# Optimization experiments

Hardware: AMD Instinct MI355X
Metric: run time of the kernel (lower is better)

Reference implementation:

```python
import jax, jax.numpy as jnp
import numpy as np

N, E, DIN, HID, HEADS = 50000, 1600000, 256, 256, 4
C = (HID // 2) // HEADS  # 32 per-head channels; HEADS*C = HID//2 per direction
NEG_SLOPE = 0.2
BN_EPS = 1e-5


def setup_inputs() -> dict:
    key = jax.random.key(0)
    ks = jax.random.split(key, 16)
    s = lambda k, shp: (jax.random.normal(k, shp, jnp.float32) * 0.05)
    return {
        "x": jax.random.normal(ks[0], (N, DIN), jnp.float32),
        "edge_index": jax.random.randint(ks[1], (2, E), 0, N, jnp.int32),
        # forward-direction GATConv params
        "W_f": s(ks[2], (DIN, HEADS * C)),
        "a_src_f": s(ks[3], (HEADS, C)),
        "a_dst_f": s(ks[4], (HEADS, C)),
        "b_f": jnp.zeros((HEADS * C,), jnp.float32),
        # backward-direction GATConv params
        "W_b": s(ks[5], (DIN, HEADS * C)),
        "a_src_b": s(ks[6], (HEADS, C)),
        "a_dst_b": s(ks[7], (HEADS, C)),
        "b_b": jnp.zeros((HEADS * C,), jnp.float32),
        # fusion linear + batchnorm (eval mode)
        "W_fuse": s(ks[8], (HID, HID)),
        "b_fuse": jnp.zeros((HID,), jnp.float32),
        "gamma": jnp.ones((HID,), jnp.float32),
        "beta": jnp.zeros((HID,), jnp.float32),
        "run_mean": jnp.zeros((HID,), jnp.float32),
        "run_var": jnp.ones((HID,), jnp.float32),
    }


def _gat(x, W, a_src, a_dst, b, src, dst):
    # x: [N, DIN]; src/dst: [E'] (self loops included)
    xl = (x @ W).reshape(N, HEADS, C)               # per-head projected features
    al = jnp.einsum("nhc,hc->nh", xl, a_src)        # [N, H]
    ar = jnp.einsum("nhc,hc->nh", xl, a_dst)        # [N, H]
    e = jax.nn.leaky_relu(al[src] + ar[dst], NEG_SLOPE)  # [E', H]
    # segment softmax over edges sharing the same destination node
    m = jax.ops.segment_max(e, dst, num_segments=N)      # [N, H]
    w = jnp.exp(e - m[dst])
    den = jax.ops.segment_sum(w, dst, num_segments=N)    # [N, H]
    alpha = w / (den[dst] + 1e-16)                       # [E', H]
    msg = xl[src] * alpha[..., None]                     # [E', H, C]
    out = jax.ops.segment_sum(msg, dst, num_segments=N)  # [N, H, C]
    return out.reshape(N, HEADS * C) + b


def reference(x, edge_index, W_f, a_src_f, a_dst_f, b_f, W_b, a_src_b, a_dst_b, b_b,
              W_fuse, b_fuse, gamma, beta, run_mean, run_var):
    loop = jnp.arange(N, dtype=edge_index.dtype)
    src = jnp.concatenate([edge_index[0], loop])  # add self loops (PyG default)
    dst = jnp.concatenate([edge_index[1], loop])
    fwd = _gat(x, W_f, a_src_f, a_dst_f, b_f, src, dst)   # [N, HID//2]
    bwd = _gat(x, W_b, a_src_b, a_dst_b, b_b, dst, src)   # reversed edges
    h = jnp.concatenate([fwd, bwd], axis=1) @ W_fuse + b_fuse  # [N, HID]
    h = (h - run_mean) * jax.lax.rsqrt(run_var + BN_EPS) * gamma + beta
    return jax.nn.relu(h)
```

## Files before the change

### kernel.cpp

```cpp
#include <hip/hip_runtime.h>

#define N_NODES 50000
#define N_EDGES 1600000
#define NEG_SLOPE 0.2f

#define NBUCK 98
#define BSH 9
#define NPB 512
#define CHUNK 6400
#define NBLK 250

typedef __attribute__((ext_vector_type(8))) short short8;
typedef __attribute__((ext_vector_type(4))) float floatx4;

__device__ __forceinline__ unsigned short f2bf(float f) {
  unsigned u = __float_as_uint(f);
  u += 0x7FFFu + ((u >> 16) & 1);
  return (unsigned short)(u >> 16);
}
__device__ __forceinline__ float bflo(unsigned u) { return __uint_as_float(u << 16); }
__device__ __forceinline__ float bfhi(unsigned u) { return __uint_as_float(u & 0xFFFF0000u); }

__global__ __launch_bounds__(256) void k_setup(
    const int* __restrict__ ei, int* __restrict__ blockhist,
    const float* __restrict__ W_f, const float* __restrict__ W_b,
    const float* __restrict__ W_fu,
    unsigned short* __restrict__ Bt1, unsigned short* __restrict__ Bt2,
    const float* __restrict__ x, unsigned short* __restrict__ Xsp)
{
  const int tid = threadIdx.x;
  if (blockIdx.x >= NBLK + 256) {
    const unsigned gid = (unsigned)(blockIdx.x - (NBLK + 256)) * 256u + tid;
    const unsigned row = gid >> 6, c = (gid & 63) * 4;
    float4 v = *(const float4*)(x + (size_t)row * 256 + c);
    unsigned short h0 = f2bf(v.x), h1 = f2bf(v.y), h2 = f2bf(v.z), h3 = f2bf(v.w);
    float l0 = v.x - __uint_as_float((unsigned)h0 << 16);
    float l1 = v.y - __uint_as_float((unsigned)h1 << 16);
    float l2 = v.z - __uint_as_float((unsigned)h2 << 16);
    float l3 = v.w - __uint_as_float((unsigned)h3 << 16);
    *(ushort4*)(Xsp + (size_t)row * 512 + c) = make_ushort4(h0, h1, h2, h3);
    *(ushort4*)(Xsp + (size_t)row * 512 + 256 + c) =
        make_ushort4(f2bf(l0), f2bf(l1), f2bf(l2), f2bf(l3));
    return;
  }
  if (blockIdx.x >= NBLK) {
    const int k = blockIdx.x - NBLK;
    float w1 = (tid < 128) ? W_f[k * 128 + tid] : W_b[k * 128 + (tid - 128)];
    Bt1[(size_t)tid * 256 + k] = f2bf(w1);
    Bt2[(size_t)tid * 256 + k] = f2bf(W_fu[k * 256 + tid]);
    return;
  }
  __shared__ int hist[2 * NBUCK];
  const int blk = blockIdx.x;
  for (int i = tid; i < 2 * NBUCK; i += 256) hist[i] = 0;
  __syncthreads();
  const int e0 = blk * CHUNK;
  for (int e = e0 + tid; e < e0 + CHUNK; e += 256) {
    int s = ei[e];
    int d = ei[N_EDGES + e];
    atomicAdd(&hist[d >> BSH], 1);
    atomicAdd(&hist[NBUCK + (s >> BSH)], 1);
  }
  __syncthreads();
  for (int i = tid; i < 2 * NBUCK; i += 256)
    blockhist[i * NBLK + blk] = hist[i];
}

__global__ __launch_bounds__(256) void k_rowscan(const int* __restrict__ blockhist,
                                                 int* __restrict__ blockoffs, int* __restrict__ bucktotal) {
  const int i = blockIdx.x;
  const int t = threadIdx.x;
  __shared__ int s[256];
  int v = (t < NBLK) ? blockhist[i * NBLK + t] : 0;
  s[t] = v;
  __syncthreads();
  for (int off = 1; off < 256; off <<= 1) {
    int u = (t >= off) ? s[t - off] : 0;
    __syncthreads();
    s[t] += u;
    __syncthreads();
  }
  if (t < NBLK) blockoffs[i * NBLK + t] = s[t] - v;
  if (t == 255) bucktotal[i] = s[255];
}

__global__ __launch_bounds__(256) void k_buckscan(const int* __restrict__ bucktotal,
                                                  int* __restrict__ buckbase, int* rpf, int* rpb) {
  __shared__ int s[256];
  const int t = threadIdx.x;
  int v = (t < 2 * NBUCK) ? bucktotal[t] : 0;
  s[t] = v;
  __syncthreads();
  for (int off = 1; off < 256; off <<= 1) {
    int u = (t >= off) ? s[t - off] : 0;
    __syncthreads();
    s[t] += u;
    __syncthreads();
  }
  if (t < 2 * NBUCK) {
    const int dir = (t >= NBUCK) ? 1 : 0;
    const int b = t - dir * NBUCK;
    const int sub = dir ? s[NBUCK - 1] : 0;
    buckbase[dir * (NBUCK + 1) + b] = s[t] - v - sub;
    if (b == NBUCK - 1) buckbase[dir * (NBUCK + 1) + NBUCK] = s[t] - sub;
  }
  if (t == 0) { rpf[N_NODES] = N_EDGES + N_NODES; rpb[N_NODES] = N_EDGES + N_NODES; }
}

__global__ __launch_bounds__(256) void k_stage(const int* __restrict__ ei,
                                               const int* __restrict__ blockoffs,
                                               const int* __restrict__ buckbase,
                                               uint2* __restrict__ staging) {
  __shared__ int cur[2 * NBUCK];
  const int blk = blockIdx.x, tid = threadIdx.x;
  for (int i = tid; i < 2 * NBUCK; i += 256) {
    int dir = (i >= NBUCK) ? 1 : 0;
    int b = i - dir * NBUCK;
    cur[i] = blockoffs[i * NBLK + blk] + buckbase[dir * (NBUCK + 1) + b];
  }
  __syncthreads();
  uint2* st0 = staging;
  uint2* st1 = staging + N_EDGES;
  const int e0 = blk * CHUNK;
  for (int e = e0 + tid; e < e0 + CHUNK; e += 256) {
    int s = ei[e];
    int d = ei[N_EDGES + e];
    int p = atomicAdd(&cur[d >> BSH], 1);
    st0[p] = make_uint2((unsigned)d, (unsigned)s);
    int q = atomicAdd(&cur[NBUCK + (s >> BSH)], 1);
    st1[q] = make_uint2((unsigned)s, (unsigned)d);
  }
}

__global__ __launch_bounds__(512) void k_bin(const uint2* __restrict__ staging,
                                             const int* __restrict__ buckbase,
                                             int* __restrict__ rpf, int* __restrict__ rpb,
                                             int* __restrict__ adjf, int* __restrict__ adjb) {
  const int b = blockIdx.x, dir = blockIdx.y, tid = threadIdx.x;
  const int node0 = b << BSH;
  const int nn = min(NPB, N_NODES - node0);
  const uint2* st = staging + (size_t)dir * N_EDGES;
  int* rp  = dir ? rpb : rpf;
  int* adj = dir ? adjb : adjf;
  const int beg = buckbase[dir * (NBUCK + 1) + b];
  const int end = buckbase[dir * (NBUCK + 1) + b + 1];

  __shared__ int cnt[NPB];
  __shared__ int wpart[8];
  cnt[tid] = 0;
  __syncthreads();
  for (int jj = beg + tid; jj < end; jj += 512)
    atomicAdd(&cnt[st[jj].x - node0], 1);
  __syncthreads();
  const int deg1 = (tid < nn) ? cnt[tid] + 1 : 0;
  int v = deg1;
  const int wl = tid & 63;
#pragma unroll
  for (int off = 1; off < 64; off <<= 1) {
    int u = __shfl_up(v, off, 64);
    if (wl >= off) v += u;
  }
  if (wl == 63) wpart[tid >> 6] = v;
  __syncthreads();
  int pre = 0;
#pragma unroll
  for (int w = 0; w < 7; ++w)
    if (w < (tid >> 6)) pre += wpart[w];
  const int excl = v + pre - deg1;
  if (tid < nn) {
    int r = beg + node0 + excl;
    rp[node0 + tid] = r;
    adj[r] = node0 + tid;
    cnt[tid] = r + 1;
  }
  __syncthreads();
  for (int jj = beg + tid; jj < end; jj += 512) {
    uint2 kv = st[jj];
    int p = atomicAdd(&cnt[kv.x - node0], 1);
    adj[p] = (int)kv.y;
  }
}

#define LDA 40

__global__ __launch_bounds__(256) void k_mm(
    const unsigned short* __restrict__ A, int M,
    const unsigned short* __restrict__ Bt,
    unsigned short* __restrict__ D0, unsigned short* __restrict__ D1,
    float* __restrict__ Df, int mode,
    const float* __restrict__ bias, const float* __restrict__ gamma,
    const float* __restrict__ beta, const float* __restrict__ mean,
    const float* __restrict__ var)
{
  __shared__ __align__(16) unsigned short As[128 * LDA];
  __shared__ __align__(16) unsigned short Bs[128 * LDA];
  const int tid = threadIdx.x;
  const int m0 = blockIdx.x * 128, col0 = blockIdx.y * 128;
  const int wave = tid >> 6, lane = tid & 63;
  const int wm = wave >> 1, wn = wave & 1;
  const int lm = lane & 15, quad = lane >> 4;

  floatx4 acc[4][4];
#pragma unroll
  for (int i = 0; i < 4; ++i)
#pragma unroll
    for (int j = 0; j < 4; ++j) acc[i][j] = (floatx4){0.f, 0.f, 0.f, 0.f};

  for (int it = 0; it < 16; ++it) {
    const int kk0 = it * 32;
    const int kbase = kk0 & 255;
    __syncthreads();
#pragma unroll
    for (int q = 0; q < 2; ++q) {
      int idx = q * 256 + tid;
      int r = idx >> 2, c8 = (idx & 3) * 8;
      ulonglong2 z; z.x = 0; z.y = 0;
      if (m0 + r < M) z = *(const ulonglong2*)(A + (size_t)(m0 + r) * 512 + kk0 + c8);
      *(ulonglong2*)&As[r * LDA + c8] = z;
    }
#pragma unroll
    for (int q = 0; q < 2; ++q) {
      int idx = q * 256 + tid;
      int nc = idx >> 2, c8 = (idx & 3) * 8;
      ulonglong2 z = *(const ulonglong2*)(Bt + (size_t)(col0 + nc) * 256 + kbase + c8);
      *(ulonglong2*)&Bs[nc * LDA + c8] = z;
    }
    __syncthreads();
    short8 a[4], b[4];
#pragma unroll
    for (int i = 0; i < 4; ++i)
      a[i] = *(const short8*)&As[(wm * 64 + i * 16 + lm) * LDA + quad * 8];
#pragma unroll
    for (int j = 0; j < 4; ++j)
      b[j] = *(const short8*)&Bs[(wn * 64 + j * 16 + lm) * LDA + quad * 8];
#pragma unroll
    for (int i = 0; i < 4; ++i)
#pragma unroll
      for (int j = 0; j < 4; ++j)
        acc[i][j] = __builtin_amdgcn_mfma_f32_16x16x32_bf16(a[i], b[j], acc[i][j], 0, 0, 0);
  }

  if (mode == 0) {
    unsigned short* C = (col0 >= 128) ? D1 : D0;
#pragma unroll
    for (int i = 0; i < 4; ++i) {
#pragma unroll
      for (int j = 0; j < 4; ++j) {
        int lc = (wn * 64 + j * 16 + lm);
#pragma unroll
        for (int reg = 0; reg < 4; ++reg) {
          int gr = m0 + wm * 64 + i * 16 + quad * 4 + reg;
          if (gr < M) C[(size_t)gr * 128 + lc] = f2bf(acc[i][j][reg]);
        }
      }
    }
  } else {
#pragma unroll
    for (int j = 0; j < 4; ++j) {
      int gc = col0 + wn * 64 + j * 16 + lm;
      float bi = bias[gc], mu = mean[gc], iv = rsqrtf(var[gc] + 1e-5f);
      float ga = gamma[gc], be = beta[gc];
#pragma unroll
      for (int i = 0; i < 4; ++i) {
#pragma unroll
        for (int reg = 0; reg < 4; ++reg) {
          int gr = m0 + wm * 64 + i * 16 + quad * 4 + reg;
          if (gr < M) {
            float v = acc[i][j][reg] + bi;
            v = (v - mu) * iv * ga + be;
            Df[(size_t)gr * 256 + gc] = fmaxf(v, 0.f);
          }
        }
      }
    }
  }
}

__global__ __launch_bounds__(256) void k_scores(
    const unsigned short* __restrict__ Xf, const unsigned short* __restrict__ Xb,
    const float* __restrict__ asf, const float* __restrict__ adf,
    const float* __restrict__ asb, const float* __restrict__ adb,
    float* __restrict__ ALf, float* __restrict__ ARf,
    float* __restrict__ ALb, float* __restrict__ ARb)
{
  const int wave = threadIdx.x >> 6, lane = threadIdx.x & 63;
  const int n = blockIdx.x * 4 + wave;
  const int hh = lane >> 5;
  const int c = lane & 31;
  float v0 = bflo((unsigned)Xf[(size_t)n * 128 + lane]);
  float v1 = bflo((unsigned)Xf[(size_t)n * 128 + 64 + lane]);
  float v2 = bflo((unsigned)Xb[(size_t)n * 128 + lane]);
  float v3 = bflo((unsigned)Xb[(size_t)n * 128 + 64 + lane]);
  float s0 = v0 * asf[hh * 32 + c],       d0 = v0 * adf[hh * 32 + c];
  float s1 = v1 * asf[(2 + hh) * 32 + c], d1 = v1 * adf[(2 + hh) * 32 + c];
  float s2 = v2 * asb[hh * 32 + c],       d2 = v2 * adb[hh * 32 + c];
  float s3 = v3 * asb[(2 + hh) * 32 + c], d3 = v3 * adb[(2 + hh) * 32 + c];
#pragma unroll
  for (int off = 16; off > 0; off >>= 1) {
    s0 += __shfl_xor(s0, off, 32); d0 += __shfl_xor(d0, off, 32);
    s1 += __shfl_xor(s1, off, 32); d1 += __shfl_xor(d1, off, 32);
    s2 += __shfl_xor(s2, off, 32); d2 += __shfl_xor(d2, off, 32);
    s3 += __shfl_xor(s3, off, 32); d3 += __shfl_xor(d3, off, 32);
  }
  if (c == 0) {
    ALf[n * 4 + hh] = s0;     ARf[n * 4 + hh] = d0;
    ALf[n * 4 + 2 + hh] = s1; ARf[n * 4 + 2 + hh] = d1;
    ALb[n * 4 + hh] = s2;     ARb[n * 4 + hh] = d2;
    ALb[n * 4 + 2 + hh] = s3; ARb[n * 4 + 2 + hh] = d3;
  }
}

__global__ __launch_bounds__(256) void k_agg(
    const uint2* __restrict__ Xf, const uint2* __restrict__ Xb,
    const int* __restrict__ rpf, const int* __restrict__ adjf,
    const int* __restrict__ rpb, const int* __restrict__ adjb,
    const float* __restrict__ ALf, const float* __restrict__ ARf,
    const float* __restrict__ ALb, const float* __restrict__ ARb,
    const float* __restrict__ bf, const float* __restrict__ bb,
    unsigned* __restrict__ Hsp)
{
  const int dir = blockIdx.y;
  const int wave = threadIdx.x >> 6;
  const int n = blockIdx.x * 4 + wave;
  const uint2* X = dir ? Xb : Xf;
  const int* rp  = dir ? rpb : rpf;
  const int* adj = dir ? adjb : adjf;
  const float* AL = dir ? ALb : ALf;
  const float* AR = dir ? ARb : ARf;
  const float* bias = dir ? bb : bf;
  const int lane = threadIdx.x & 63;
  const int sub = lane >> 5;
  const int t = lane & 31;
  const unsigned h = (unsigned)(t >> 3);
  const float arn = AR[((unsigned)n << 2) | h];
  const int beg = rp[n], end = rp[n + 1];
  const int iters = (end - beg + 1) >> 1;
  const int endm1 = end - 1;
  float a0 = 0.f, a1 = 0.f, a2 = 0.f, a3 = 0.f, den = 0.f;
  int j = beg + sub;
#pragma unroll 4
  for (int it = 0; it < iters; ++it, j += 2) {
    int jj = min(j, endm1);
    int nb = adj[jj];
    float al = AL[((unsigned)nb << 2) | h];
    uint2 u = X[(unsigned)nb * 32u + (unsigned)t];
    float e = al + arn;
    e = fmaxf(e, e * NEG_SLOPE);
    float w = __expf(e);
    w = (j <= endm1) ? w : 0.f;
    den += w;
    a0 = fmaf(w, bflo(u.x), a0);
    a1 = fmaf(w, bfhi(u.x), a1);
    a2 = fmaf(w, bflo(u.y), a2);
    a3 = fmaf(w, bfhi(u.y), a3);
  }
  a0 += __shfl_xor(a0, 32); a1 += __shfl_xor(a1, 32);
  a2 += __shfl_xor(a2, 32); a3 += __shfl_xor(a3, 32);
  den += __shfl_xor(den, 32);
  if (sub == 0) {
    float inv = 1.f / (den + 1e-16f);
    float4 bv = *(const float4*)(bias + 4 * t);
    float v0 = a0 * inv + bv.x, v1 = a1 * inv + bv.y;
    float v2 = a2 * inv + bv.z, v3 = a3 * inv + bv.w;
    unsigned short h0 = f2bf(v0), h1 = f2bf(v1), h2 = f2bf(v2), h3 = f2bf(v3);
    float l0 = v0 - __uint_as_float((unsigned)h0 << 16);
    float l1 = v1 - __uint_as_float((unsigned)h1 << 16);
    float l2 = v2 - __uint_as_float((unsigned)h2 << 16);
    float l3 = v3 - __uint_as_float((unsigned)h3 << 16);
    uint2 hiw, low;
    hiw.x = ((unsigned)h1 << 16) | h0;
    hiw.y = ((unsigned)h3 << 16) | h2;
    low.x = ((unsigned)f2bf(l1) << 16) | f2bf(l0);
    low.y = ((unsigned)f2bf(l3) << 16) | f2bf(l2);
    unsigned base = (unsigned)n * 256u + (unsigned)dir * 64u + 2u * (unsigned)t;
    *(uint2*)(Hsp + base) = hiw;
    *(uint2*)(Hsp + base + 128u) = low;
  }
}


extern "C" void kernel_launch(void* const* d_in, const int* in_sizes, int n_in,
                              void* d_out, int out_size, void* d_ws, size_t ws_size,
                              hipStream_t stream) {
  const float* x    = (const float*)d_in[0];
  const int*   ei   = (const int*)d_in[1];
  const float* W_f  = (const float*)d_in[2];
  const float* asf  = (const float*)d_in[3];
  const float* adf  = (const float*)d_in[4];
  const float* b_f  = (const float*)d_in[5];
  const float* W_b  = (const float*)d_in[6];
  const float* asb  = (const float*)d_in[7];
  const float* adb  = (const float*)d_in[8];
  const float* b_b  = (const float*)d_in[9];
  const float* W_fu = (const float*)d_in[10];
  const float* b_fu = (const float*)d_in[11];
  const float* gam  = (const float*)d_in[12];
  const float* bet  = (const float*)d_in[13];
  const float* mean = (const float*)d_in[14];
  const float* var  = (const float*)d_in[15];
  float* out = (float*)d_out;

  char* base = (char*)d_ws;
  size_t off = 0;
  auto alloc = [&](size_t bytes) {
    void* p = base + off;
    off = (off + bytes + 255) & ~(size_t)255;
    return p;
  };
  unsigned* Hsp          = (unsigned*)alloc((size_t)N_NODES * 256 * 4);
  unsigned short* Xsp    = (unsigned short*)Hsp;
  unsigned short* Xf     = (unsigned short*)alloc((size_t)N_NODES * 128 * 2);
  unsigned short* Xb     = (unsigned short*)alloc((size_t)N_NODES * 128 * 2);
  unsigned short* Bt1    = (unsigned short*)alloc((size_t)256 * 256 * 2);
  unsigned short* Bt2    = (unsigned short*)alloc((size_t)256 * 256 * 2);
  float* ALf  = (float*)alloc((size_t)N_NODES * 4 * 4);
  float* ARf  = (float*)alloc((size_t)N_NODES * 4 * 4);
  float* ALb  = (float*)alloc((size_t)N_NODES * 4 * 4);
  float* ARb  = (float*)alloc((size_t)N_NODES * 4 * 4);
  int* rpf    = (int*)alloc((size_t)(N_NODES + 1) * 4);
  int* rpb    = (int*)alloc((size_t)(N_NODES + 1) * 4);
  int* adjf   = (int*)alloc((size_t)(N_EDGES + N_NODES) * 4);
  int* adjb   = (int*)alloc((size_t)(N_EDGES + N_NODES) * 4);
  int* blockhist = (int*)alloc((size_t)2 * NBUCK * NBLK * 4);
  int* blockoffs = (int*)alloc((size_t)2 * NBUCK * NBLK * 4);
  int* bucktotal = (int*)alloc((size_t)2 * NBUCK * 4);
  int* buckbase  = (int*)alloc((size_t)2 * (NBUCK + 1) * 4);
  uint2* staging = (uint2*)alloc((size_t)2 * N_EDGES * 8);
  (void)ws_size; (void)in_sizes; (void)n_in; (void)out_size;

  const int SPLITB = (N_NODES * 64) / 256;
  k_setup<<<NBLK + 256 + SPLITB, 256, 0, stream>>>(ei, blockhist, W_f, W_b, W_fu,
                                                   Bt1, Bt2, x, Xsp);
  k_rowscan<<<2 * NBUCK, 256, 0, stream>>>(blockhist, blockoffs, bucktotal);
  k_buckscan<<<1, 256, 0, stream>>>(bucktotal, buckbase, rpf, rpb);
  k_stage<<<NBLK, 256, 0, stream>>>(ei, blockoffs, buckbase, staging);
  k_bin<<<dim3(NBUCK, 2), 512, 0, stream>>>(staging, buckbase, rpf, rpb, adjf, adjb);

  const int MB = (N_NODES + 127) / 128;
  k_mm<<<dim3(MB, 2), 256, 0, stream>>>(Xsp, N_NODES, Bt1, Xf, Xb, nullptr, 0,
                                        nullptr, nullptr, nullptr, nullptr, nullptr);
  k_scores<<<N_NODES / 4, 256, 0, stream>>>(Xf, Xb, asf, adf, asb, adb,
                                            ALf, ARf, ALb, ARb);
  k_agg<<<dim3(N_NODES / 4, 2), 256, 0, stream>>>((const uint2*)Xf, (const uint2*)Xb,
                                                  rpf, adjf, rpb, adjb,
                                                  ALf, ARf, ALb, ARb, b_f, b_b, Hsp);
  k_mm<<<dim3(MB, 2), 256, 0, stream>>>((const unsigned short*)Hsp, N_NODES, Bt2,
                                        nullptr, nullptr, out, 1,
                                        b_fu, gam, bet, mean, var);
}
```

Measured before the change: 430.1 us.

## Drop split-bf16 hi/lo operands, pack staging records, use exp2 in aggregation

Both GEMMs previously used a split bf16 representation (hi plus residual lo, K=512) for X and the aggregated hidden state. Now they use a single bf16 copy with K=256, which halves the matmul loop and the bytes written and read. The edge staging buffer now packs the local node index and neighbour into one 32-bit word instead of a uint2, halving scatter traffic. Attention scores are prescaled by log2(e) so the aggregation can use exp2f, and the odd-edge tail is peeled out of the main loop. The cost is lower precision in both matmuls, and the 16-bit neighbour field relies on node ids staying below 65536.

```diff
diff --git a/kernel.cpp b/kernel.cpp
--- a/kernel.cpp
+++ b/kernel.cpp
@@ -3,6 +3,7 @@
 #define N_NODES 50000
 #define N_EDGES 1600000
 #define NEG_SLOPE 0.2f
+#define LOG2E 1.44269504f
 
 #define NBUCK 98
 #define BSH 9
@@ -26,21 +27,15 @@
     const float* __restrict__ W_f, const float* __restrict__ W_b,
     const float* __restrict__ W_fu,
     unsigned short* __restrict__ Bt1, unsigned short* __restrict__ Bt2,
-    const float* __restrict__ x, unsigned short* __restrict__ Xsp)
+    const float* __restrict__ x, unsigned short* __restrict__ Xb16)
 {
   const int tid = threadIdx.x;
   if (blockIdx.x >= NBLK + 256) {
     const unsigned gid = (unsigned)(blockIdx.x - (NBLK + 256)) * 256u + tid;
     const unsigned row = gid >> 6, c = (gid & 63) * 4;
     float4 v = *(const float4*)(x + (size_t)row * 256 + c);
-    unsigned short h0 = f2bf(v.x), h1 = f2bf(v.y), h2 = f2bf(v.z), h3 = f2bf(v.w);
-    float l0 = v.x - __uint_as_float((unsigned)h0 << 16);
-    float l1 = v.y - __uint_as_float((unsigned)h1 << 16);
-    float l2 = v.z - __uint_as_float((unsigned)h2 << 16);
-    float l3 = v.w - __uint_as_float((unsigned)h3 << 16);
-    *(ushort4*)(Xsp + (size_t)row * 512 + c) = make_ushort4(h0, h1, h2, h3);
-    *(ushort4*)(Xsp + (size_t)row * 512 + 256 + c) =
-        make_ushort4(f2bf(l0), f2bf(l1), f2bf(l2), f2bf(l3));
+    *(ushort4*)(Xb16 + (size_t)row * 256 + c) =
+        make_ushort4(f2bf(v.x), f2bf(v.y), f2bf(v.z), f2bf(v.w));
     return;
   }
   if (blockIdx.x >= NBLK) {
@@ -110,7 +105,7 @@
 __global__ __launch_bounds__(256) void k_stage(const int* __restrict__ ei,
                                                const int* __restrict__ blockoffs,
                                                const int* __restrict__ buckbase,
-                                               uint2* __restrict__ staging) {
+                                               unsigned* __restrict__ staging) {
   __shared__ int cur[2 * NBUCK];
   const int blk = blockIdx.x, tid = threadIdx.x;
   for (int i = tid; i < 2 * NBUCK; i += 256) {
@@ -119,27 +114,27 @@
     cur[i] = blockoffs[i * NBLK + blk] + buckbase[dir * (NBUCK + 1) + b];
   }
   __syncthreads();
-  uint2* st0 = staging;
-  uint2* st1 = staging + N_EDGES;
+  unsigned* st0 = staging;
+  unsigned* st1 = staging + N_EDGES;
   const int e0 = blk * CHUNK;
   for (int e = e0 + tid; e < e0 + CHUNK; e += 256) {
     int s = ei[e];
     int d = ei[N_EDGES + e];
     int p = atomicAdd(&cur[d >> BSH], 1);
-    st0[p] = make_uint2((unsigned)d, (unsigned)s);
+    st0[p] = ((unsigned)(d & (NPB - 1)) << 16) | (unsigned)s;
     int q = atomicAdd(&cur[NBUCK + (s >> BSH)], 1);
-    st1[q] = make_uint2((unsigned)s, (unsigned)d);
-  }
-}
-
-__global__ __launch_bounds__(512) void k_bin(const uint2* __restrict__ staging,
+    st1[q] = ((unsigned)(s & (NPB - 1)) << 16) | (unsigned)d;
+  }
+}
+
+__global__ __launch_bounds__(512) void k_bin(const unsigned* __restrict__ staging,
                                              const int* __restrict__ buckbase,
                                              int* __restrict__ rpf, int* __restrict__ rpb,
                                              int* __restrict__ adjf, int* __restrict__ adjb) {
   const int b = blockIdx.x, dir = blockIdx.y, tid = threadIdx.x;
   const int node0 = b << BSH;
   const int nn = min(NPB, N_NODES - node0);
-  const uint2* st = staging + (size_t)dir * N_EDGES;
+  const unsigned* st = staging + (size_t)dir * N_EDGES;
   int* rp  = dir ? rpb : rpf;
   int* adj = dir ? adjb : adjf;
   const int beg = buckbase[dir * (NBUCK + 1) + b];
@@ -150,7 +145,7 @@
   cnt[tid] = 0;
   __syncthreads();
   for (int jj = beg + tid; jj < end; jj += 512)
-    atomicAdd(&cnt[st[jj].x - node0], 1);
+    atomicAdd(&cnt[st[jj] >> 16], 1);
   __syncthreads();
   const int deg1 = (tid < nn) ? cnt[tid] + 1 : 0;
   int v = deg1;
@@ -175,9 +170,9 @@
   }
   __syncthreads();
   for (int jj = beg + tid; jj < end; jj += 512) {
-    uint2 kv = st[jj];
-    int p = atomicAdd(&cnt[kv.x - node0], 1);
-    adj[p] = (int)kv.y;
+    unsigned rec = st[jj];
+    int p = atomicAdd(&cnt[rec >> 16], 1);
+    adj[p] = (int)(rec & 0xFFFFu);
   }
 }
 
@@ -206,23 +201,22 @@
 #pragma unroll
     for (int j = 0; j < 4; ++j) acc[i][j] = (floatx4){0.f, 0.f, 0.f, 0.f};
 
-  for (int it = 0; it < 16; ++it) {
+  for (int it = 0; it < 8; ++it) {
     const int kk0 = it * 32;
-    const int kbase = kk0 & 255;
     __syncthreads();
 #pragma unroll
     for (int q = 0; q < 2; ++q) {
       int idx = q * 256 + tid;
       int r = idx >> 2, c8 = (idx & 3) * 8;
       ulonglong2 z; z.x = 0; z.y = 0;
-      if (m0 + r < M) z = *(const ulonglong2*)(A + (size_t)(m0 + r) * 512 + kk0 + c8);
+      if (m0 + r < M) z = *(const ulonglong2*)(A + (size_t)(m0 + r) * 256 + kk0 + c8);
       *(ulonglong2*)&As[r * LDA + c8] = z;
     }
 #pragma unroll
     for (int q = 0; q < 2; ++q) {
       int idx = q * 256 + tid;
       int nc = idx >> 2, c8 = (idx & 3) * 8;
-      ulonglong2 z = *(const ulonglong2*)(Bt + (size_t)(col0 + nc) * 256 + kbase + c8);
+      ulonglong2 z = *(const ulonglong2*)(Bt + (size_t)(col0 + nc) * 256 + kk0 + c8);
       *(ulonglong2*)&Bs[nc * LDA + c8] = z;
     }
     __syncthreads();
@@ -303,10 +297,10 @@
     s3 += __shfl_xor(s3, off, 32); d3 += __shfl_xor(d3, off, 32);
   }
   if (c == 0) {
-    ALf[n * 4 + hh] = s0;     ARf[n * 4 + hh] = d0;
-    ALf[n * 4 + 2 + hh] = s1; ARf[n * 4 + 2 + hh] = d1;
-    ALb[n * 4 + hh] = s2;     ARb[n * 4 + hh] = d2;
-    ALb[n * 4 + 2 + hh] = s3; ARb[n * 4 + 2 + hh] = d3;
+    ALf[n * 4 + hh] = s0 * LOG2E;     ARf[n * 4 + hh] = d0 * LOG2E;
+    ALf[n * 4 + 2 + hh] = s1 * LOG2E; ARf[n * 4 + 2 + hh] = d1 * LOG2E;
+    ALb[n * 4 + hh] = s2 * LOG2E;     ARb[n * 4 + hh] = d2 * LOG2E;
+    ALb[n * 4 + 2 + hh] = s3 * LOG2E; ARb[n * 4 + 2 + hh] = d3 * LOG2E;
   }
 }
 
@@ -317,7 +311,7 @@
     const float* __restrict__ ALf, const float* __restrict__ ARf,
     const float* __restrict__ ALb, const float* __restrict__ ARb,
     const float* __restrict__ bf, const float* __restrict__ bb,
-    unsigned* __restrict__ Hsp)
+    unsigned* __restrict__ H16)
 {
   const int dir = blockIdx.y;
   const int wave = threadIdx.x >> 6;
@@ -330,24 +324,36 @@
   const float* bias = dir ? bb : bf;
   const int lane = threadIdx.x & 63;
   const int sub = lane >> 5;
-  const int t = lane & 31;
-  const unsigned h = (unsigned)(t >> 3);
+  const unsigned t = (unsigned)(lane & 31);
+  const unsigned h = t >> 3;
   const float arn = AR[((unsigned)n << 2) | h];
   const int beg = rp[n], end = rp[n + 1];
-  const int iters = (end - beg + 1) >> 1;
-  const int endm1 = end - 1;
+  const int cntE = end - beg;
+  const int full = cntE >> 1;
   float a0 = 0.f, a1 = 0.f, a2 = 0.f, a3 = 0.f, den = 0.f;
-  int j = beg + sub;
+  const int* ap = adj + beg + sub;
 #pragma unroll 4
-  for (int it = 0; it < iters; ++it, j += 2) {
-    int jj = min(j, endm1);
-    int nb = adj[jj];
+  for (int it = 0; it < full; ++it, ap += 2) {
+    int nb = *ap;
     float al = AL[((unsigned)nb << 2) | h];
-    uint2 u = X[(unsigned)nb * 32u + (unsigned)t];
-    float e = al + arn;
-    e = fmaxf(e, e * NEG_SLOPE);
-    float w = __expf(e);
-    w = (j <= endm1) ? w : 0.f;
+    uint2 u = X[((unsigned)nb << 5) | t];
+    float s = al + arn;
+    float e = fmaxf(s, s * NEG_SLOPE);
+    float w = exp2f(e);
+    den += w;
+    a0 = fmaf(w, bflo(u.x), a0);
+    a1 = fmaf(w, bfhi(u.x), a1);
+    a2 = fmaf(w, bflo(u.y), a2);
+    a3 = fmaf(w, bfhi(u.y), a3);
+  }
+  if (cntE & 1) {
+    int nb = adj[end - 1];
+    float al = AL[((unsigned)nb << 2) | h];
+    uint2 u = X[((unsigned)nb << 5) | t];
+    float s = al + arn;
+    float e = fmaxf(s, s * NEG_SLOPE);
+    float w = exp2f(e);
+    w = (sub == 0) ? w : 0.f;
     den += w;
     a0 = fmaf(w, bflo(u.x), a0);
     a1 = fmaf(w, bfhi(u.x), a1);
@@ -362,19 +368,11 @@
     float4 bv = *(const float4*)(bias + 4 * t);
     float v0 = a0 * inv + bv.x, v1 = a1 * inv + bv.y;
     float v2 = a2 * inv + bv.z, v3 = a3 * inv + bv.w;
-    unsigned short h0 = f2bf(v0), h1 = f2bf(v1), h2 = f2bf(v2), h3 = f2bf(v3);
-    float l0 = v0 - __uint_as_float((unsigned)h0 << 16);
-    float l1 = v1 - __uint_as_float((unsigned)h1 << 16);
-    float l2 = v2 - __uint_as_float((unsigned)h2 << 16);
-    float l3 = v3 - __uint_as_float((unsigned)h3 << 16);
-    uint2 hiw, low;
-    hiw.x = ((unsigned)h1 << 16) | h0;
-    hiw.y = ((unsigned)h3 << 16) | h2;
-    low.x = ((unsigned)f2bf(l1) << 16) | f2bf(l0);
-    low.y = ((unsigned)f2bf(l3) << 16) | f2bf(l2);
-    unsigned base = (unsigned)n * 256u + (unsigned)dir * 64u + 2u * (unsigned)t;
-    *(uint2*)(Hsp + base) = hiw;
-    *(uint2*)(Hsp + base + 128u) = low;
+    uint2 hw;
+    hw.x = ((unsigned)f2bf(v1) << 16) | f2bf(v0);
+    hw.y = ((unsigned)f2bf(v3) << 16) | f2bf(v2);
+    unsigned base = (unsigned)n * 128u + (unsigned)dir * 64u + 2u * t;
+    *(uint2*)(H16 + base) = hw;
   }
 }
 
@@ -407,12 +405,12 @@
     off = (off + bytes + 255) & ~(size_t)255;
     return p;
   };
-  unsigned* Hsp          = (unsigned*)alloc((size_t)N_NODES * 256 * 4);
-  unsigned short* Xsp    = (unsigned short*)Hsp;
-  unsigned short* Xf     = (unsigned short*)alloc((size_t)N_NODES * 128 * 2);
-  unsigned short* Xb     = (unsigned short*)alloc((size_t)N_NODES * 128 * 2);
-  unsigned short* Bt1    = (unsigned short*)alloc((size_t)256 * 256 * 2);
-  unsigned short* Bt2    = (unsigned short*)alloc((size_t)256 * 256 * 2);
+  unsigned short* Xb16 = (unsigned short*)alloc((size_t)N_NODES * 256 * 2);
+  unsigned* H16        = (unsigned*)Xb16;
+  unsigned short* Xf   = (unsigned short*)alloc((size_t)N_NODES * 128 * 2);
+  unsigned short* Xb   = (unsigned short*)alloc((size_t)N_NODES * 128 * 2);
+  unsigned short* Bt1  = (unsigned short*)alloc((size_t)256 * 256 * 2);
+  unsigned short* Bt2  = (unsigned short*)alloc((size_t)256 * 256 * 2);
   float* ALf  = (float*)alloc((size_t)N_NODES * 4 * 4);
   float* ARf  = (float*)alloc((size_t)N_NODES * 4 * 4);
   float* ALb  = (float*)alloc((size_t)N_NODES * 4 * 4);
@@ -425,26 +423,26 @@
   int* blockoffs = (int*)alloc((size_t)2 * NBUCK * NBLK * 4);
   int* bucktotal = (int*)alloc((size_t)2 * NBUCK * 4);
   int* buckbase  = (int*)alloc((size_t)2 * (NBUCK + 1) * 4);
-  uint2* staging = (uint2*)alloc((size_t)2 * N_EDGES * 8);
+  unsigned* staging = (unsigned*)alloc((size_t)2 * N_EDGES * 4);
   (void)ws_size; (void)in_sizes; (void)n_in; (void)out_size;
 
-  const int SPLITB = (N_NODES * 64) / 256;
-  k_setup<<<NBLK + 256 + SPLITB, 256, 0, stream>>>(ei, blockhist, W_f, W_b, W_fu,
-                                                   Bt1, Bt2, x, Xsp);
+  const int XB = (N_NODES * 64) / 256;
+  k_setup<<<NBLK + 256 + XB, 256, 0, stream>>>(ei, blockhist, W_f, W_b, W_fu,
+                                               Bt1, Bt2, x, Xb16);
   k_rowscan<<<2 * NBUCK, 256, 0, stream>>>(blockhist, blockoffs, bucktotal);
   k_buckscan<<<1, 256, 0, stream>>>(bucktotal, buckbase, rpf, rpb);
   k_stage<<<NBLK, 256, 0, stream>>>(ei, blockoffs, buckbase, staging);
   k_bin<<<dim3(NBUCK, 2), 512, 0, stream>>>(staging, buckbase, rpf, rpb, adjf, adjb);
 
   const int MB = (N_NODES + 127) / 128;
-  k_mm<<<dim3(MB, 2), 256, 0, stream>>>(Xsp, N_NODES, Bt1, Xf, Xb, nullptr, 0,
+  k_mm<<<dim3(MB, 2), 256, 0, stream>>>(Xb16, N_NODES, Bt1, Xf, Xb, nullptr, 0,
                                         nullptr, nullptr, nullptr, nullptr, nullptr);
   k_scores<<<N_NODES / 4, 256, 0, stream>>>(Xf, Xb, asf, adf, asb, adb,
                                             ALf, ARf, ALb, ARb);
   k_agg<<<dim3(N_NODES / 4, 2), 256, 0, stream>>>((const uint2*)Xf, (const uint2*)Xb,
                                                   rpf, adjf, rpb, adjb,
-                                                  ALf, ARf, ALb, ARb, b_f, b_b, Hsp);
-  k_mm<<<dim3(MB, 2), 256, 0, stream>>>((const unsigned short*)Hsp, N_NODES, Bt2,
+                                                  ALf, ARf, ALb, ARb, b_f, b_b, H16);
+  k_mm<<<dim3(MB, 2), 256, 0, stream>>>((const unsigned short*)H16, N_NODES, Bt2,
                                         nullptr, nullptr, out, 1,
                                         b_fu, gam, bet, mean, var);
 }
```

New measurement: 383.1 us. -10.9%, faster.
